# Performance work log

Measured on AMD Instinct MI355X. Metric: run time of the kernel, lower is better.

Reference implementation:

```python
import jax, jax.numpy as jnp
import numpy as np

N = 50000      # nodes
E = 1_600_000  # edges
DIN, HID, OUT, H = 128, 32, 32, 4


def _glorot(key, shape):
    fan_in, fan_out = shape[0], shape[1] if len(shape) > 1 else shape[0]
    s = jnp.sqrt(6.0 / (fan_in + fan_out)).astype(jnp.float32)
    return jax.random.uniform(key, shape, jnp.float32, -s, s)


def setup_inputs() -> dict:
    key = jax.random.key(0)
    ks = jax.random.split(key, 16)
    inp = {
        "x": jax.random.normal(ks[0], (N, DIN), jnp.float32),
        "edge_index": jax.random.randint(ks[1], (2, E), 0, N, dtype=jnp.int32),
        "edge_weight": jax.random.uniform(ks[2], (E, 1), jnp.float32),
        # layer 1: in=DIN, heads=H, out=HID, concat=True
        "Wl1": _glorot(ks[3], (DIN, H * HID)),
        "Wr1": _glorot(ks[4], (DIN, H * HID)),
        "We1": _glorot(ks[5], (1, H * HID)),
        "att1": _glorot(ks[6], (H, HID)),
        "b1": jnp.zeros((H * HID,), jnp.float32),
        # layer 2: in=H*HID, heads=H, out=OUT, concat=False (mean over heads)
        "Wl2": _glorot(ks[7], (H * HID, H * OUT)),
        "Wr2": _glorot(ks[8], (H * HID, H * OUT)),
        "We2": _glorot(ks[9], (1, H * OUT)),
        "att2": _glorot(ks[10], (H, OUT)),
        "b2": jnp.zeros((OUT,), jnp.float32),
    }
    return inp


def gatv2_layer(x, edge_index, edge_weight, Wl, Wr, We, att, b, concat):
    """Faithful PyG GATv2Conv (share_weights=False, negative_slope=0.2,
    add_self_loops=True with fill_value='mean' for edge_attr)."""
    n = x.shape[0]
    heads, c = att.shape
    src, dst = edge_index[0], edge_index[1]
    # add self loops with mean edge weight (PyG default when edge_dim is set)
    loop = jnp.arange(n, dtype=edge_index.dtype)
    src = jnp.concatenate([src, loop])
    dst = jnp.concatenate([dst, loop])
    ew = jnp.concatenate(
        [edge_weight, jnp.full((n, edge_weight.shape[1]), jnp.mean(edge_weight), edge_weight.dtype)], axis=0)

    xl = (x @ Wl).reshape(n, heads, c)   # source transform (lin_l)
    xr = (x @ Wr).reshape(n, heads, c)   # target transform (lin_r)
    e_feat = (ew @ We).reshape(-1, heads, c)

    z = jax.nn.leaky_relu(xl[src] + xr[dst] + e_feat, 0.2)   # [E', H, C]
    logits = jnp.einsum('ehc,hc->eh', z, att)                # [E', H]

    # segment softmax over incoming edges of each target node
    m = jax.ops.segment_max(logits, dst, num_segments=n)
    m = jnp.where(jnp.isfinite(m), m, 0.0)
    p = jnp.exp(logits - m[dst])
    denom = jax.ops.segment_sum(p, dst, num_segments=n)
    alpha = p / (denom[dst] + 1e-16)                          # [E', H]

    out = jax.ops.segment_sum(xl[src] * alpha[..., None], dst, num_segments=n)  # [N, H, C]
    out = out.reshape(n, heads * c) if concat else out.mean(axis=1)
    return out + b


def reference(x, edge_index, edge_weight, Wl1, Wr1, We1, att1, b1,
              Wl2, Wr2, We2, att2, b2):
    h = gatv2_layer(x, edge_index, edge_weight, Wl1, Wr1, We1, att1, b1, concat=True)
    h = jax.nn.elu(h)
    out = gatv2_layer(h, edge_index, edge_weight, Wl2, Wr2, We2, att2, b2, concat=False)
    return out
```

## Files before the change

kernel.cpp:

```cpp
#include <hip/hip_runtime.h>
#include <hip/hip_fp16.h>
#include <math.h>
#include <type_traits>


typedef _Float16 half8 __attribute__((ext_vector_type(8)));
typedef float floatx4 __attribute__((ext_vector_type(4)));

__global__ __launch_bounds__(256) void bucket_hist_sum(
    const int* __restrict__ dst, const float* __restrict__ ew,
    int* __restrict__ bcnt, float* __restrict__ sumbuf, int E) {
    __shared__ int h[256];
    h[threadIdx.x] = 0;
    __syncthreads();
    float s = 0.f;
    for (int i = blockIdx.x * blockDim.x + threadIdx.x; i < E; i += gridDim.x * blockDim.x) {
        atomicAdd(&h[dst[i] >> 8], 1);
        s += ew[i];
    }
#pragma unroll
    for (int off = 1; off <= 32; off <<= 1)
        s += __shfl_xor(s, off, 64);
    if ((threadIdx.x & 63) == 0)
        atomicAdd(sumbuf, s);
    __syncthreads();
    int v = h[threadIdx.x];
    if (v) atomicAdd(&bcnt[threadIdx.x], v);
}

__global__ void bucket_scan(const int* __restrict__ bcnt, int* __restrict__ bbase,
                            int* __restrict__ bcur, int NBK) {
    __shared__ int sh[256];
    int t = threadIdx.x;
    int v = (t < NBK) ? bcnt[t] : 0;
    sh[t] = v;
    __syncthreads();
    for (int off = 1; off < 256; off <<= 1) {
        int y = 0;
        if (t >= off) y = sh[t - off];
        __syncthreads();
        sh[t] += y;
        __syncthreads();
    }
    int ex = sh[t] - v;
    if (t <= NBK) bbase[t] = ex;
    if (t < NBK) bcur[t] = ex;
}

__global__ __launch_bounds__(256) void partition_kernel(
    const int* __restrict__ src, const int* __restrict__ dst, const float* __restrict__ ew,
    int* __restrict__ bcur, int2* __restrict__ srec, int E) {
    __shared__ int h[256];
    __shared__ int gb[256];
    const int t = threadIdx.x;
    h[t] = 0;
    __syncthreads();
    const int base = blockIdx.x * 2048;
    int d[8], sv[8];
    float wv[8];
#pragma unroll
    for (int j = 0; j < 8; j++) {
        int i = base + t + j * 256;
        if (i < E) {
            d[j] = dst[i];
            sv[j] = src[i];
            wv[j] = ew[i];
            atomicAdd(&h[d[j] >> 8], 1);
        } else {
            d[j] = -1;
        }
    }
    __syncthreads();
    int cntt = h[t];
    if (cntt) gb[t] = atomicAdd(&bcur[t], cntt);
    h[t] = 0;
    __syncthreads();
#pragma unroll
    for (int j = 0; j < 8; j++) {
        if (d[j] >= 0) {
            int b = d[j] >> 8;
            int r = atomicAdd(&h[b], 1);
            int pos = gb[b] + r;
            srec[pos] = make_int2(sv[j] | ((d[j] & 255) << 20), __float_as_int(wv[j]));
        }
    }
}

__global__ __launch_bounds__(1024) void dst_hist_kernel(
    const int2* __restrict__ srec, const int* __restrict__ bbase,
    int* __restrict__ cnt, int N) {
    __shared__ int h4[4][256];
    const int t = threadIdx.x;
    const int grp = t >> 8, sub = t & 255;
    h4[grp][sub] = 0;
    __syncthreads();
    const int b = blockIdx.x;
    const int e0 = bbase[b], e1 = bbase[b + 1];
    for (int i = e0 + t; i < e1; i += 1024)
        atomicAdd(&h4[grp][(srec[i].x >> 20) & 255], 1);
    __syncthreads();
    if (t < 256) {
        int node = (b << 8) + t;
        if (node < N) cnt[node] = h4[0][t] + h4[1][t] + h4[2][t] + h4[3][t];
    }
}

__global__ void scan1_kernel(const int* __restrict__ cnt, int* __restrict__ rowp,
                             int* __restrict__ bsum, int N) {
    __shared__ int sh[256];
    int i = blockIdx.x * 256 + threadIdx.x;
    int v = (i < N) ? (cnt[i] + 1) : 0;
    sh[threadIdx.x] = v;
    __syncthreads();
    for (int off = 1; off < 256; off <<= 1) {
        int y = 0;
        if ((int)threadIdx.x >= off) y = sh[threadIdx.x - off];
        __syncthreads();
        sh[threadIdx.x] += y;
        __syncthreads();
    }
    int incl = sh[threadIdx.x];
    if (i < N) rowp[i] = incl - v;
    if (threadIdx.x == 255) bsum[blockIdx.x] = incl;
}

__global__ void scan2_kernel(int* __restrict__ bsum, int nb) {
    __shared__ int sh[256];
    int v = ((int)threadIdx.x < nb) ? bsum[threadIdx.x] : 0;
    sh[threadIdx.x] = v;
    __syncthreads();
    for (int off = 1; off < 256; off <<= 1) {
        int y = 0;
        if ((int)threadIdx.x >= off) y = sh[threadIdx.x - off];
        __syncthreads();
        sh[threadIdx.x] += y;
        __syncthreads();
    }
    int incl = sh[threadIdx.x];
    if ((int)threadIdx.x < nb) bsum[threadIdx.x] = incl - v;
}

__global__ void scan3_kernel(int* __restrict__ rowp, const int* __restrict__ bsum,
                             const int* __restrict__ cnt, const float* __restrict__ sumbuf,
                             int2* __restrict__ crec, int N, int E) {
    int i = blockIdx.x * 256 + threadIdx.x;
    if (i < N) {
        int rp = rowp[i] + bsum[blockIdx.x];
        rowp[i] = rp;
        crec[rp + cnt[i]] = make_int2(i, __float_as_int(sumbuf[0] * (1.0f / (float)E)));
    }
    if (i == 0) rowp[N] = E + N;
}

__global__ __launch_bounds__(1024) void refine_kernel(
    const int2* __restrict__ srec, const int* __restrict__ bbase,
    const int* __restrict__ rowp, int2* __restrict__ crec, int N) {
    __shared__ int cur[256];
    const int t = threadIdx.x;
    const int b = blockIdx.x;
    if (t < 256) {
        int node = (b << 8) + t;
        cur[t] = (node < N) ? rowp[node] : 0;
    }
    __syncthreads();
    const int e0 = bbase[b], e1 = bbase[b + 1];
    for (int i = e0 + t; i < e1; i += 1024) {
        int2 rec = srec[i];
        int dlow = (rec.x >> 20) & 255;
        int pos = atomicAdd(&cur[dlow], 1);
        crec[pos] = make_int2(rec.x & 0xFFFFF, rec.y);
    }
}

__global__ __launch_bounds__(256) void prep_w2_kernel(
    const float* __restrict__ Wa1, const float* __restrict__ Wb1,
    const float* __restrict__ Wa2, const float* __restrict__ Wb2,
    _Float16* __restrict__ Wh1, _Float16* __restrict__ Wh2,
    int* __restrict__ bcnt) {
    const int bid = blockIdx.x;
    if (bid == 0 && threadIdx.x < 260) bcnt[threadIdx.x] = 0;
    const int sel = bid >> 7;
    const float* Wa = sel ? Wa2 : Wa1;
    const float* Wb = sel ? Wb2 : Wb1;
    _Float16* Wh = sel ? Wh2 : Wh1;
    int tid = (bid & 127) * 256 + threadIdx.x;
    int j = tid & 7;
    int lane = (tid >> 3) & 63;
    int f = tid >> 9;
    int kk = f & 3;
    int ct = f >> 2;
    int col = ct * 16 + (lane & 15);
    int k = kk * 32 + ((lane >> 4) << 3) + j;
    float v = (col < 128) ? Wa[k * 128 + col] : Wb[k * 128 + (col - 128)];
    Wh[tid] = (_Float16)v;
}

template <typename T>
__global__ __launch_bounds__(256) void gemm_mfma_kernel(
    const T* __restrict__ X, const _Float16* __restrict__ Wh,
    __half* __restrict__ Yh, float* __restrict__ Yb, int N) {
    __shared__ _Float16 Xs[64 * 128];
    const int tid = threadIdx.x;
    const int lane = tid & 63;
    const int w = tid >> 6;
    const int rb = blockIdx.x * 64;

    half8 wf[4][4];
#pragma unroll
    for (int ct = 0; ct < 4; ct++)
#pragma unroll
        for (int kk = 0; kk < 4; kk++)
            wf[ct][kk] = *(const half8*)(Wh + (size_t)(((w * 4 + ct) * 4 + kk) * 512 + lane * 8));

    if constexpr (std::is_same<T, float>::value) {
#pragma unroll
        for (int it = 0; it < 8; it++) {
            int c = it * 256 + tid;
            int row = c >> 5;
            int f4 = c & 31;
            float4 v = make_float4(0.f, 0.f, 0.f, 0.f);
            if (rb + row < N)
                v = ((const float4*)X)[(size_t)(rb + row) * 32 + f4];
            _Float16 h[4] = {(_Float16)v.x, (_Float16)v.y, (_Float16)v.z, (_Float16)v.w};
            int byteoff = row * 256 + ((f4 * 8) ^ ((row & 7) << 4));
            *(uint2*)((char*)Xs + byteoff) = *(uint2*)h;
        }
    } else {
#pragma unroll
        for (int it = 0; it < 4; it++) {
            int c = it * 256 + tid;
            int row = c >> 4;
            int f16 = c & 15;
            int4 v = make_int4(0, 0, 0, 0);
            if (rb + row < N)
                v = ((const int4*)X)[(size_t)(rb + row) * 16 + f16];
            int byteoff = row * 256 + ((f16 * 16) ^ ((row & 7) << 4));
            *(int4*)((char*)Xs + byteoff) = v;
        }
    }
    __syncthreads();

    floatx4 acc[4][4];
#pragma unroll
    for (int ct = 0; ct < 4; ct++)
#pragma unroll
        for (int rt = 0; rt < 4; rt++)
            acc[ct][rt] = (floatx4){0.f, 0.f, 0.f, 0.f};

#pragma unroll
    for (int kk = 0; kk < 4; kk++) {
        half8 xf[4];
#pragma unroll
        for (int rt = 0; rt < 4; rt++) {
            int row = rt * 16 + (lane & 15);
            int kb = kk * 64 + ((lane >> 4) << 4);
            int off = row * 256 + (kb ^ ((row & 7) << 4));
            xf[rt] = *(const half8*)((const char*)Xs + off);
        }
#pragma unroll
        for (int ct = 0; ct < 4; ct++)
#pragma unroll
            for (int rt = 0; rt < 4; rt++)
                acc[ct][rt] = __builtin_amdgcn_mfma_f32_16x16x32_f16(
                    wf[ct][kk], xf[rt], acc[ct][rt], 0, 0, 0);
    }

    const int rsub = lane & 15;
    const int c4 = (lane >> 4) << 2;
#pragma unroll
    for (int ct = 0; ct < 4; ct++) {
        int gct = w * 4 + ct;
#pragma unroll
        for (int rt = 0; rt < 4; rt++) {
            int row = rb + rt * 16 + rsub;
            if (row < N) {
                floatx4 a = acc[ct][rt];
                if (gct < 8) {
                    int col = gct * 16 + c4;
                    __half2 hp[2];
                    hp[0] = __floats2half2_rn(a[0], a[1]);
                    hp[1] = __floats2half2_rn(a[2], a[3]);
                    *(uint2*)(Yh + (size_t)row * 128 + col) = *(uint2*)hp;
                } else {
                    int col = (gct - 8) * 16 + c4;
                    *(float4*)(Yb + (size_t)row * 128 + col) =
                        make_float4(a[0], a[1], a[2], a[3]);
                }
            }
        }
    }
}

template <int CTRL>
__device__ __forceinline__ float dpp_sum_step(float v) {
    int t = __builtin_amdgcn_update_dpp(0, __float_as_int(v), CTRL, 0xF, 0xF, true);
    return v + __int_as_float(t);
}

__device__ __forceinline__ float2 cvt_h2(unsigned u) {
    __half2 h = *(__half2*)&u;
    return __half22float2(h);
}

__global__ __launch_bounds__(256) void agg_kernel(
    const __half* __restrict__ xlh, const float* __restrict__ xr,
    const int* __restrict__ rowp, const int2* __restrict__ crec,
    const float* __restrict__ We, const float* __restrict__ att, const float* __restrict__ bias,
    void* __restrict__ out, int N, int mode) {
    const int wid = threadIdx.x >> 6;
    const int lane = threadIdx.x & 63;
    const int n = blockIdx.x * 4 + wid;
    if (n >= N) return;
    const int g = lane >> 4;
    const int q = lane & 15;
    const int c0 = q << 3;
    const float LOG2E = 1.4426950408889634f;

    float we[8], xv[8], at6[8], at4[8];
    {
        float4 wA = *(const float4*)(We + c0);
        float4 wB = *(const float4*)(We + c0 + 4);
        we[0]=wA.x; we[1]=wA.y; we[2]=wA.z; we[3]=wA.w;
        we[4]=wB.x; we[5]=wB.y; we[6]=wB.z; we[7]=wB.w;
        float4 rA = *(const float4*)(xr + (size_t)n * 128 + c0);
        float4 rB = *(const float4*)(xr + (size_t)n * 128 + c0 + 4);
        xv[0]=rA.x; xv[1]=rA.y; xv[2]=rA.z; xv[3]=rA.w;
        xv[4]=rB.x; xv[5]=rB.y; xv[6]=rB.z; xv[7]=rB.w;
        float4 aA = *(const float4*)(att + c0);
        float4 aB = *(const float4*)(att + c0 + 4);
        float av[8] = {aA.x, aA.y, aA.z, aA.w, aB.x, aB.y, aB.z, aB.w};
#pragma unroll
        for (int c = 0; c < 8; c++) {
            at6[c] = 0.6f * LOG2E * av[c];
            at4[c] = 0.4f * LOG2E * av[c];
        }
    }

    float acc[8];
#pragma unroll
    for (int c = 0; c < 8; c++) acc[c] = 0.f;
    float l0 = 0.f;

    const int e0 = __builtin_amdgcn_readfirstlane(rowp[n]);
    const int e1 = __builtin_amdgcn_readfirstlane(rowp[n + 1]);
    const int cnt = e1 - e0;
    const int T = (cnt + 3) >> 2;

    auto recload = [&](int i) -> int2 {
        int idx = e0 + (i << 2) + g;
        idx = (idx < e1 - 1) ? idx : (e1 - 1);
        return crec[idx];
    };
    auto gatherx = [&](int s) -> int4 {
        return *(const int4*)(xlh + (size_t)s * 128 + c0);
    };
    auto process = [&](int4 xh, float w, bool valid) {
        float2 x01 = cvt_h2(xh.x), x23 = cvt_h2(xh.y);
        float2 x45 = cvt_h2(xh.z), x67 = cvt_h2(xh.w);
        float xs[8] = {x01.x, x01.y, x23.x, x23.y, x45.x, x45.y, x67.x, x67.y};
        float p = 0.f;
#pragma unroll
        for (int c = 0; c < 8; c++) {
            float z = xs[c] + fmaf(w, we[c], xv[c]);
            p = fmaf(at6[c], z, fmaf(at4[c], fabsf(z), p));
        }
        p = dpp_sum_step<0xB1>(p);
        p = dpp_sum_step<0x4E>(p);
        float qe = valid ? __builtin_amdgcn_exp2f(p) : 0.f;
        l0 += qe;
#pragma unroll
        for (int c = 0; c < 8; c++) acc[c] = fmaf(qe, xs[c], acc[c]);
    };

    int2 r0 = recload(0), r1 = recload(1), r2 = recload(2), r3 = recload(3);
    int4 x0 = gatherx(r0.x), x1 = gatherx(r1.x);
    for (int i = 0; i < T; ++i) {
        int2 r4 = recload(i + 4);
        int4 x2 = gatherx(r2.x);
        process(x0, __int_as_float(r0.y), (e0 + (i << 2) + g) < e1);
        r0 = r1; r1 = r2; r2 = r3; r3 = r4;
        x0 = x1; x1 = x2;
    }

    l0 += __shfl_xor(l0, 16, 64);
    l0 += __shfl_xor(l0, 32, 64);
#pragma unroll
    for (int c = 0; c < 8; c++) {
        acc[c] += __shfl_xor(acc[c], 16, 64);
        acc[c] += __shfl_xor(acc[c], 32, 64);
    }
    float rdenom = 1.0f / (l0 + 1e-16f);
    float r[8];
#pragma unroll
    for (int c = 0; c < 8; c++) r[c] = acc[c] * rdenom;

    if (mode == 0) {
        if (g == 0) {
            float4 bA = *(const float4*)(bias + c0);
            float4 bB = *(const float4*)(bias + c0 + 4);
            float bv[8] = {bA.x, bA.y, bA.z, bA.w, bB.x, bB.y, bB.z, bB.w};
            float o[8];
#pragma unroll
            for (int c = 0; c < 8; c++) {
                float v = r[c] + bv[c];
                o[c] = (v > 0.f) ? v : (__expf(v) - 1.f);
            }
            __half2 p0 = __floats2half2_rn(o[0], o[1]);
            __half2 p1 = __floats2half2_rn(o[2], o[3]);
            __half2 p2 = __floats2half2_rn(o[4], o[5]);
            __half2 p3 = __floats2half2_rn(o[6], o[7]);
            int4 pk = make_int4(*(int*)&p0, *(int*)&p1, *(int*)&p2, *(int*)&p3);
            *(int4*)((__half*)out + (size_t)n * 128 + c0) = pk;
        }
    } else {
#pragma unroll
        for (int c = 0; c < 8; c++) {
            r[c] += __shfl_xor(r[c], 4, 64);
            r[c] += __shfl_xor(r[c], 8, 64);
        }
        if (lane < 4) {
            int w0 = lane << 3;
            float4 bA = *(const float4*)(bias + w0);
            float4 bB = *(const float4*)(bias + w0 + 4);
            float bv[8] = {bA.x, bA.y, bA.z, bA.w, bB.x, bB.y, bB.z, bB.w};
            float o[8];
#pragma unroll
            for (int c = 0; c < 8; c++) o[c] = 0.25f * r[c] + bv[c];
            float* op = (float*)out + (size_t)n * 32 + w0;
            *(float4*)op       = make_float4(o[0], o[1], o[2], o[3]);
            *(float4*)(op + 4) = make_float4(o[4], o[5], o[6], o[7]);
        }
    }
}

extern "C" void kernel_launch(void* const* d_in, const int* in_sizes, int n_in,
                              void* d_out, int out_size, void* d_ws, size_t ws_size,
                              hipStream_t stream) {
    const float* x    = (const float*)d_in[0];
    const int*  eidx  = (const int*)d_in[1];
    const float* ew   = (const float*)d_in[2];
    const float* Wl1  = (const float*)d_in[3];
    const float* Wr1  = (const float*)d_in[4];
    const float* We1  = (const float*)d_in[5];
    const float* att1 = (const float*)d_in[6];
    const float* b1   = (const float*)d_in[7];
    const float* Wl2  = (const float*)d_in[8];
    const float* Wr2  = (const float*)d_in[9];
    const float* We2  = (const float*)d_in[10];
    const float* att2 = (const float*)d_in[11];
    const float* b2   = (const float*)d_in[12];

    const int N = in_sizes[0] / 128;
    const int E = in_sizes[1] / 2;
    const int* src = eidx;
    const int* dst = eidx + E;
    const int NBK = (N + 255) >> 8;

    char* p = (char*)d_ws;
    auto alloc = [&](size_t bytes) -> void* {
        void* r = (void*)p;
        p += (bytes + 255) & ~(size_t)255;
        return r;
    };
    __half* xlh   = (__half*)alloc((size_t)N * 128 * sizeof(__half));
    float* xr     = (float*)alloc((size_t)N * 128 * sizeof(float));
    __half* h1h   = (__half*)alloc((size_t)N * 128 * sizeof(float));
    int2*  crec   = (int2*)alloc((size_t)(E + N + 64) * sizeof(int2));
    int*   rowp   = (int*)alloc((size_t)(N + 1) * sizeof(int));
    int*   cnt    = (int*)alloc((size_t)N * sizeof(int));
    int*   bcnt   = (int*)alloc(260 * sizeof(int));
    float* sumbuf = (float*)(bcnt + 256);
    int*   bbase  = (int*)alloc(260 * sizeof(int));
    int*   bcur   = (int*)alloc(260 * sizeof(int));
    int*   bsum   = (int*)alloc(256 * sizeof(int));
    _Float16* Wh1 = (_Float16*)alloc(32768 * sizeof(_Float16));
    _Float16* Wh2 = (_Float16*)alloc(32768 * sizeof(_Float16));
    int2*  srec   = (int2*)h1h;

    prep_w2_kernel<<<256, 256, 0, stream>>>(Wl1, Wr1, Wl2, Wr2, Wh1, Wh2, bcnt);

    bucket_hist_sum<<<1024, 256, 0, stream>>>(dst, ew, bcnt, sumbuf, E);
    bucket_scan<<<1, 256, 0, stream>>>(bcnt, bbase, bcur, NBK);
    partition_kernel<<<(E + 2047) / 2048, 256, 0, stream>>>(src, dst, ew, bcur, srec, E);
    dst_hist_kernel<<<NBK, 1024, 0, stream>>>(srec, bbase, cnt, N);

    int nb = (N + 255) / 256;
    scan1_kernel<<<nb, 256, 0, stream>>>(cnt, rowp, bsum, N);
    scan2_kernel<<<1, 256, 0, stream>>>(bsum, nb);
    scan3_kernel<<<nb, 256, 0, stream>>>(rowp, bsum, cnt, sumbuf, crec, N, E);

    refine_kernel<<<NBK, 1024, 0, stream>>>(srec, bbase, rowp, crec, N);

    gemm_mfma_kernel<float><<<(N + 63) / 64, 256, 0, stream>>>(x, Wh1, xlh, xr, N);
    agg_kernel<<<(N + 3) / 4, 256, 0, stream>>>(xlh, xr, rowp, crec,
                                                We1, att1, b1, (void*)h1h, N, 0);
    gemm_mfma_kernel<_Float16><<<(N + 63) / 64, 256, 0, stream>>>(
        (const _Float16*)h1h, Wh2, xlh, xr, N);
    agg_kernel<<<(N + 3) / 4, 256, 0, stream>>>(xlh, xr, rowp, crec,
                                                We2, att2, b2, d_out, N, 1);
}
```

Baseline: 364.5 us.

## Fuse bucket scan and degree histogram into partition, merge scan2 into scan3

```diff
diff --git a/kernel.cpp b/kernel.cpp
--- a/kernel.cpp
+++ b/kernel.cpp
@@ -28,31 +28,28 @@
     if (v) atomicAdd(&bcnt[threadIdx.x], v);
 }
 
-__global__ void bucket_scan(const int* __restrict__ bcnt, int* __restrict__ bbase,
-                            int* __restrict__ bcur, int NBK) {
-    __shared__ int sh[256];
-    int t = threadIdx.x;
-    int v = (t < NBK) ? bcnt[t] : 0;
-    sh[t] = v;
-    __syncthreads();
-    for (int off = 1; off < 256; off <<= 1) {
-        int y = 0;
-        if (t >= off) y = sh[t - off];
-        __syncthreads();
-        sh[t] += y;
-        __syncthreads();
-    }
-    int ex = sh[t] - v;
-    if (t <= NBK) bbase[t] = ex;
-    if (t < NBK) bcur[t] = ex;
-}
-
 __global__ __launch_bounds__(256) void partition_kernel(
     const int* __restrict__ src, const int* __restrict__ dst, const float* __restrict__ ew,
-    int* __restrict__ bcur, int2* __restrict__ srec, int E) {
+    const int* __restrict__ bcnt, int* __restrict__ bcur, int* __restrict__ bbase,
+    int* __restrict__ cnt, int2* __restrict__ srec, int E, int NBK) {
+    __shared__ int ex[256];
     __shared__ int h[256];
     __shared__ int gb[256];
     const int t = threadIdx.x;
+
+    int v = (t < NBK) ? bcnt[t] : 0;
+    ex[t] = v;
+    __syncthreads();
+    for (int off = 1; off < 256; off <<= 1) {
+        int y = 0;
+        if (t >= off) y = ex[t - off];
+        __syncthreads();
+        ex[t] += y;
+        __syncthreads();
+    }
+    const int exbase = ex[t] - v;
+    if (blockIdx.x == 0 && t <= NBK) bbase[t] = exbase;
+
     h[t] = 0;
     __syncthreads();
     const int base = blockIdx.x * 2048;
@@ -66,13 +63,14 @@
             sv[j] = src[i];
             wv[j] = ew[i];
             atomicAdd(&h[d[j] >> 8], 1);
+            atomicAdd(&cnt[d[j]], 1);
         } else {
             d[j] = -1;
         }
     }
     __syncthreads();
     int cntt = h[t];
-    if (cntt) gb[t] = atomicAdd(&bcur[t], cntt);
+    if (cntt) gb[t] = exbase + atomicAdd(&bcur[t], cntt);
     h[t] = 0;
     __syncthreads();
 #pragma unroll
@@ -86,25 +84,6 @@
     }
 }
 
-__global__ __launch_bounds__(1024) void dst_hist_kernel(
-    const int2* __restrict__ srec, const int* __restrict__ bbase,
-    int* __restrict__ cnt, int N) {
-    __shared__ int h4[4][256];
-    const int t = threadIdx.x;
-    const int grp = t >> 8, sub = t & 255;
-    h4[grp][sub] = 0;
-    __syncthreads();
-    const int b = blockIdx.x;
-    const int e0 = bbase[b], e1 = bbase[b + 1];
-    for (int i = e0 + t; i < e1; i += 1024)
-        atomicAdd(&h4[grp][(srec[i].x >> 20) & 255], 1);
-    __syncthreads();
-    if (t < 256) {
-        int node = (b << 8) + t;
-        if (node < N) cnt[node] = h4[0][t] + h4[1][t] + h4[2][t] + h4[3][t];
-    }
-}
-
 __global__ void scan1_kernel(const int* __restrict__ cnt, int* __restrict__ rowp,
                              int* __restrict__ bsum, int N) {
     __shared__ int sh[256];
@@ -124,28 +103,25 @@
     if (threadIdx.x == 255) bsum[blockIdx.x] = incl;
 }
 
-__global__ void scan2_kernel(int* __restrict__ bsum, int nb) {
+__global__ void scan3_kernel(int* __restrict__ rowp, const int* __restrict__ bsum,
+                             const int* __restrict__ cnt, const float* __restrict__ sumbuf,
+                             int2* __restrict__ crec, int N, int E, int nb) {
     __shared__ int sh[256];
-    int v = ((int)threadIdx.x < nb) ? bsum[threadIdx.x] : 0;
-    sh[threadIdx.x] = v;
+    const int t = threadIdx.x;
+    int v = (t < nb) ? bsum[t] : 0;
+    sh[t] = v;
     __syncthreads();
     for (int off = 1; off < 256; off <<= 1) {
         int y = 0;
-        if ((int)threadIdx.x >= off) y = sh[threadIdx.x - off];
-        __syncthreads();
-        sh[threadIdx.x] += y;
-        __syncthreads();
-    }
-    int incl = sh[threadIdx.x];
-    if ((int)threadIdx.x < nb) bsum[threadIdx.x] = incl - v;
-}
-
-__global__ void scan3_kernel(int* __restrict__ rowp, const int* __restrict__ bsum,
-                             const int* __restrict__ cnt, const float* __restrict__ sumbuf,
-                             int2* __restrict__ crec, int N, int E) {
-    int i = blockIdx.x * 256 + threadIdx.x;
+        if (t >= off) y = sh[t - off];
+        __syncthreads();
+        sh[t] += y;
+        __syncthreads();
+    }
+    int boff = sh[blockIdx.x] - bsum[blockIdx.x];
+    int i = blockIdx.x * 256 + t;
     if (i < N) {
-        int rp = rowp[i] + bsum[blockIdx.x];
+        int rp = rowp[i] + boff;
         rowp[i] = rp;
         crec[rp + cnt[i]] = make_int2(i, __float_as_int(sumbuf[0] * (1.0f / (float)E)));
     }
@@ -176,9 +152,12 @@
     const float* __restrict__ Wa1, const float* __restrict__ Wb1,
     const float* __restrict__ Wa2, const float* __restrict__ Wb2,
     _Float16* __restrict__ Wh1, _Float16* __restrict__ Wh2,
-    int* __restrict__ bcnt) {
+    int* __restrict__ bcnt, int* __restrict__ bcur, int* __restrict__ cnt, int N) {
     const int bid = blockIdx.x;
     if (bid == 0 && threadIdx.x < 260) bcnt[threadIdx.x] = 0;
+    if (bid == 1 && threadIdx.x < 260) bcur[threadIdx.x] = 0;
+    int zi = bid * 256 + threadIdx.x;
+    if (zi < N) cnt[zi] = 0;
     const int sel = bid >> 7;
     const float* Wa = sel ? Wa2 : Wa1;
     const float* Wb = sel ? Wb2 : Wb1;
@@ -477,17 +456,16 @@
     _Float16* Wh2 = (_Float16*)alloc(32768 * sizeof(_Float16));
     int2*  srec   = (int2*)h1h;
 
-    prep_w2_kernel<<<256, 256, 0, stream>>>(Wl1, Wr1, Wl2, Wr2, Wh1, Wh2, bcnt);
+    prep_w2_kernel<<<256, 256, 0, stream>>>(Wl1, Wr1, Wl2, Wr2, Wh1, Wh2,
+                                            bcnt, bcur, cnt, N);
 
     bucket_hist_sum<<<1024, 256, 0, stream>>>(dst, ew, bcnt, sumbuf, E);
-    bucket_scan<<<1, 256, 0, stream>>>(bcnt, bbase, bcur, NBK);
-    partition_kernel<<<(E + 2047) / 2048, 256, 0, stream>>>(src, dst, ew, bcur, srec, E);
-    dst_hist_kernel<<<NBK, 1024, 0, stream>>>(srec, bbase, cnt, N);
+    partition_kernel<<<(E + 2047) / 2048, 256, 0, stream>>>(
+        src, dst, ew, bcnt, bcur, bbase, cnt, srec, E, NBK);
 
     int nb = (N + 255) / 256;
     scan1_kernel<<<nb, 256, 0, stream>>>(cnt, rowp, bsum, N);
-    scan2_kernel<<<1, 256, 0, stream>>>(bsum, nb);
-    scan3_kernel<<<nb, 256, 0, stream>>>(rowp, bsum, cnt, sumbuf, crec, N, E);
+    scan3_kernel<<<nb, 256, 0, stream>>>(rowp, bsum, cnt, sumbuf, crec, N, E, nb);
 
     refine_kernel<<<NBK, 1024, 0, stream>>>(srec, bbase, rowp, crec, N);
 
```

Result: slower. 421.8 us (+15.7%).
